# Optimization experiments

Measured on AMD Instinct MI355X. Metric: run time of the kernel, lower is better.

The kernel has to match this reference:

```python
import jax, jax.numpy as jnp
import numpy as np

# Model hyperparams (match init_kwargs)
B, T, CIN, COUT = 4, 12, 4, 4
P = 16; HIMG = WIMG = 256; HP = WP = 16
D = 384; L = 4; DFF = 4 * D; MAXG = 0.3
CPLX = jnp.complex64

# NOTE: RiemannianCliffordConv2d / TemporalPropagator / FluxTracker / basis /
# encoder / decoder sources were not provided; they are reconstructed here as
# faithful-structure surrogates: plain conv2d for the Clifford conv, complex
# linear eigen-basis encode/decode, exp-decay scan operators, complex FFN,
# patch-embed conv encoder and per-patch linear decoder. sde_mode='ode' so the
# stochastic branch is skipped, matching the explicit guard in the source.

def _ln(x, g, b):
    m = x.mean(-1, keepdims=True)
    v = jnp.var(x, axis=-1, keepdims=True)
    return (x - m) * jax.lax.rsqrt(v + 1e-5) * g + b

def _conv(x, w, b, stride, pad):
    y = jax.lax.conv_general_dilated(x, w, (stride, stride), pad,
                                     dimension_numbers=('NCHW', 'OIHW', 'NCHW'))
    return y + b[None, :, None, None]

def _pscan(A, X):
    # first-order linear recurrence h_t = A_t*h_{t-1} + X_t via associative scan over axis=1
    def comb(l, r):
        al, xl = l; ar, xr = r
        return al * ar, xl * ar + xr
    return jax.lax.associative_scan(comb, (A, X), axis=1)[1]

def _cgelu(z):
    return jax.nn.gelu(z.real) + 1j * jax.nn.gelu(z.imag)

def _model(x, dt, enc_w, enc_b, ns_g, ns_b, cw, cb, nt_g, nt_b,
           E_re, E_im, Ei_re, Ei_im, lam_flux, Ws_re, Ws_im, Wg, nu, omega,
           w1_re, w1_im, w2_re, w2_im, dec_w, dec_b):
    Bx, Tx = x.shape[0], x.shape[1]
    # ---- encoder: patch-embed conv -> complex latent (B,T,D,HP,WP)
    xf = x.reshape(Bx * Tx, CIN, HIMG, WIMG)
    e = _conv(xf, enc_w, enc_b, P, 'VALID')              # (BT, 2D, HP, WP)
    zr, zi = jnp.split(e, 2, axis=1)
    z = (zr + 1j * zi).astype(CPLX).reshape(Bx, Tx, D, HP, WP)
    for i in range(L):
        E = E_re[i] + 1j * E_im[i]
        Ei = Ei_re[i] + 1j * Ei_im[i]
        Ws = Ws_re[i] + 1j * Ws_im[i]
        W1 = w1_re[i] + 1j * w1_im[i]
        W2 = w2_re[i] + 1j * w2_im[i]
        # ---- _apply_spatial (residual Clifford conv on stacked re/im)
        xflat = z.reshape(Bx * Tx, D, HP, WP)
        xr2 = jnp.concatenate([xflat.real, xflat.imag], axis=1)   # (BT,2D,H,W)
        xn = jnp.transpose(xr2, (0, 2, 3, 1))
        xn = _ln(xn, ns_g[i], ns_b[i])
        xn = jnp.transpose(xn, (0, 3, 1, 2))
        xs = _conv(xn, cw[i], cb[i], 1, 'SAME')
        sre, sim = jnp.split(xs, 2, axis=1)
        xflat = xflat + (sre + 1j * sim)
        z = xflat.reshape(Bx, Tx, D, HP, WP)
        # ---- eigen-basis encode
        xp = jnp.transpose(z, (0, 1, 3, 4, 2))                    # (B,T,H,W,D)
        x_eig = jnp.einsum('bthwd,de->bthwe', xp, E)
        x_mean = x_eig.mean(axis=(2, 3))                          # (B,T,D)
        # ---- flux tracker scan (states start at zero => flux_prev term vanishes)
        a = jnp.exp(-jax.nn.softplus(lam_flux[i])[None, None] * dt[..., None])
        A_flux = a.astype(CPLX)
        X_flux = x_mean * dt[..., None]
        flux = _pscan(A_flux, X_flux)                             # (B,T,D) complex
        source = jnp.einsum('btd,de->bte', flux, Ws)
        gate = jax.nn.sigmoid(flux.real * Wg[i][None, None])      # (B,T,D) real
        g = gate[:, :, None, None, :]
        forcing = x_eig * g + source[:, :, None, None, :] * (1.0 - g)
        # ---- transition operators and temporal pscan
        lam = jnp.clip(-jax.nn.softplus(nu[i]), -5.0, MAXG) + 1j * omega[i]  # (D,)
        op_decay = jnp.exp(lam[None, None] * dt[..., None])       # (B,T,D) complex
        op_forcing = (op_decay - 1.0) / lam
        u_t = forcing * op_forcing[:, :, None, None, :]           # (B,T,H,W,D)
        # h_prev is zero-initialized per _init_states => its t0 contribution is zero
        A_full = jnp.broadcast_to(op_decay[:, :, None, None, :], u_t.shape)
        u_out = _pscan(A_full, u_t)                               # (B,T,H,W,D)
        # ---- decode + temporal FFN residual
        decoded = jnp.einsum('bthwd,de->bthwe', u_out, Ei)
        dec5 = jnp.transpose(decoded, (0, 1, 4, 2, 3))            # (B,T,D,H,W)
        df = dec5.reshape(Bx * Tx, D, HP, WP)
        dr = jnp.concatenate([df.real, df.imag], axis=1)
        dn = _ln(jnp.transpose(dr, (0, 2, 3, 1)), nt_g[i], nt_b[i])
        dn = jnp.transpose(dn, (0, 3, 1, 2))
        nre, nim = jnp.split(dn, 2, axis=1)
        xcl = jnp.transpose(nre + 1j * nim, (0, 2, 3, 1))          # (BT,H,W,D)
        delta = jnp.einsum('bhwf,fd->bhwd', _cgelu(jnp.einsum('bhwd,df->bhwf', xcl, W1)), W2)
        delta = jnp.transpose(delta, (0, 3, 1, 2))
        x_out = (df + delta).reshape(Bx, Tx, D, HP, WP)
        z = z + x_out
    # ---- ensemble decoder (mean member): per-patch linear head + depth-to-space
    feats = jnp.concatenate([z.real, z.imag], axis=2)             # (B,T,2D,H,W)
    fl = jnp.transpose(feats, (0, 1, 3, 4, 2))                    # (B,T,H,W,2D)
    y = jnp.einsum('bthwc,oc->bthwo', fl, dec_w) + dec_b
    y = y.reshape(Bx, Tx, HP, WP, COUT, P, P)
    y = jnp.transpose(y, (0, 1, 4, 2, 5, 3, 6)).reshape(Bx, Tx, COUT, HP * P, WP * P)
    return y


def setup_inputs() -> dict:
    key = jax.random.key(0)
    ks = jax.random.split(key, 32)
    s = 0.02
    d = {}
    d['x'] = jax.random.normal(ks[0], (B, T, CIN, HIMG, WIMG), dtype=jnp.float32)
    d['dt'] = jax.random.uniform(ks[1], (B, T), minval=0.5, maxval=1.5, dtype=jnp.float32)
    d['enc_w'] = jax.random.normal(ks[2], (2 * D, CIN, P, P), dtype=jnp.float32) * s
    d['enc_b'] = jnp.zeros((2 * D,), jnp.float32)
    d['ns_g'] = jnp.ones((L, 2 * D), jnp.float32)
    d['ns_b'] = jnp.zeros((L, 2 * D), jnp.float32)
    d['cw'] = jax.random.normal(ks[3], (L, 2 * D, 2 * D, 3, 3), dtype=jnp.float32) * s
    d['cb'] = jnp.zeros((L, 2 * D), jnp.float32)
    d['nt_g'] = jnp.ones((L, 2 * D), jnp.float32)
    d['nt_b'] = jnp.zeros((L, 2 * D), jnp.float32)
    d['E_re'] = jax.random.normal(ks[4], (L, D, D), dtype=jnp.float32) * s
    d['E_im'] = jax.random.normal(ks[5], (L, D, D), dtype=jnp.float32) * s
    d['Ei_re'] = jax.random.normal(ks[6], (L, D, D), dtype=jnp.float32) * s
    d['Ei_im'] = jax.random.normal(ks[7], (L, D, D), dtype=jnp.float32) * s
    d['lam_flux'] = jax.random.normal(ks[8], (L, D), dtype=jnp.float32)
    d['Ws_re'] = jax.random.normal(ks[9], (L, D, D), dtype=jnp.float32) * s
    d['Ws_im'] = jax.random.normal(ks[10], (L, D, D), dtype=jnp.float32) * s
    d['Wg'] = jax.random.normal(ks[11], (L, D), dtype=jnp.float32)
    d['nu'] = jax.random.normal(ks[12], (L, D), dtype=jnp.float32)
    d['omega'] = jax.random.normal(ks[13], (L, D), dtype=jnp.float32) * 0.5
    d['w1_re'] = jax.random.normal(ks[14], (L, D, DFF), dtype=jnp.float32) * s
    d['w1_im'] = jax.random.normal(ks[15], (L, D, DFF), dtype=jnp.float32) * s
    d['w2_re'] = jax.random.normal(ks[16], (L, DFF, D), dtype=jnp.float32) * s
    d['w2_im'] = jax.random.normal(ks[17], (L, DFF, D), dtype=jnp.float32) * s
    d['dec_w'] = jax.random.normal(ks[18], (COUT * P * P, 2 * D), dtype=jnp.float32) * s
    d['dec_b'] = jnp.zeros((COUT * P * P,), jnp.float32)
    return d


def reference(x, dt, enc_w, enc_b, ns_g, ns_b, cw, cb, nt_g, nt_b,
              E_re, E_im, Ei_re, Ei_im, lam_flux, Ws_re, Ws_im, Wg, nu, omega,
              w1_re, w1_im, w2_re, w2_im, dec_w, dec_b):
    return _model(x, dt, enc_w, enc_b, ns_g, ns_b, cw, cb, nt_g, nt_b,
                  E_re, E_im, Ei_re, Ei_im, lam_flux, Ws_re, Ws_im, Wg, nu, omega,
                  w1_re, w1_im, w2_re, w2_im, dec_w, dec_b)
```

## Files before the change

kernel.cpp:

```cpp
#include <hip/hip_runtime.h>
#include <cstddef>
#include <cstdint>

typedef unsigned short u16;
typedef short bf16x8 __attribute__((ext_vector_type(8)));
typedef float f32x4 __attribute__((ext_vector_type(4)));

__device__ __forceinline__ float gelu_tanh(float x) {
  float x3 = x * x * x;
  float t = tanhf(0.7978845608028654f * (x + 0.044715f * x3));
  return 0.5f * x * (1.0f + t);
}
__device__ __forceinline__ float softplus_f(float x) {
  return (x > 20.0f) ? x : log1pf(expf(x));
}
__device__ __forceinline__ u16 f2bf(float f) {
  uint32_t u = __float_as_uint(f);
  uint32_t r = (u + 0x7fffu + ((u >> 16) & 1u)) >> 16;
  return (u16)r;
}
__device__ __forceinline__ float bf2f(u16 v) {
  return __uint_as_float(((uint32_t)v) << 16);
}

__device__ __forceinline__ void gload16(const u16* g, u16* l) {
  __builtin_amdgcn_global_load_lds(
      (const __attribute__((address_space(1))) void*)g,
      (__attribute__((address_space(3))) void*)l, 16, 0, 0);
}

template <int TN, int MODE>
__global__ __launch_bounds__(256) void gemm_kernel(
    const u16* __restrict__ A, const u16* __restrict__ Bt, int K, int ldc,
    float* __restrict__ Cf, u16* __restrict__ Cb,
    const float* __restrict__ bias, const u16* __restrict__ Db) {
  static_assert(TN == 64, "192x64 tile only");
  __shared__ u16 As[2][192 * 32];
  __shared__ u16 Bs[2][64 * 32];
  const int m0 = blockIdx.x * 192, n0 = blockIdx.y * 64;
  const int tid = threadIdx.x;
  const int lane = tid & 63, w = tid >> 6;
  const int lane15 = lane & 15, quad = lane >> 4;
  const int r0 = lane >> 2, e0 = (lane & 3) * 8;

  const u16* ag0 = A + (size_t)(m0 + w * 48 + r0) * K + e0;
  const u16* ag1 = ag0 + (size_t)16 * K;
  const u16* ag2 = ag0 + (size_t)32 * K;
  const u16* bg0 = Bt + (size_t)(n0 + w * 16 + r0) * K + e0;

  f32x4 acc[3][4] = {};
  const int abase = (w * 48 + lane15) * 32 + quad * 8;
  const int bbase = lane15 * 32 + quad * 8;

  for (int k0 = 0; k0 < K; k0 += 64) {
#pragma unroll
    for (int p = 0; p < 2; ++p) {
      const int kk = k0 + 32 * p;
      gload16(ag0 + kk, &As[p][(w * 48) * 32]);
      gload16(ag1 + kk, &As[p][(w * 48 + 16) * 32]);
      gload16(ag2 + kk, &As[p][(w * 48 + 32) * 32]);
      gload16(bg0 + kk, &Bs[p][(w * 16) * 32]);
    }
    __syncthreads();
#pragma unroll
    for (int p = 0; p < 2; ++p) {
      bf16x8 af[3], bf[4];
#pragma unroll
      for (int i = 0; i < 3; ++i) af[i] = *(const bf16x8*)&As[p][abase + i * 16 * 32];
#pragma unroll
      for (int j = 0; j < 4; ++j) bf[j] = *(const bf16x8*)&Bs[p][bbase + j * 16 * 32];
#pragma unroll
      for (int i = 0; i < 3; ++i)
#pragma unroll
        for (int j = 0; j < 4; ++j)
          acc[i][j] = __builtin_amdgcn_mfma_f32_16x16x32_bf16(af[i], bf[j], acc[i][j], 0, 0, 0);
    }
    __syncthreads();
  }

  const int mw = m0 + w * 48;
#pragma unroll
  for (int i = 0; i < 3; ++i) {
#pragma unroll
    for (int j = 0; j < 4; ++j) {
      const int col = n0 + j * 16 + lane15;
#pragma unroll
      for (int r = 0; r < 4; ++r) {
        const int row = mw + i * 16 + quad * 4 + r;
        const float v = acc[i][j][r];
        const size_t idx = (size_t)row * ldc + col;
        if (MODE == 0) {
          Cf[idx] = v;
        } else if (MODE == 1) {
          Cb[idx] = f2bf(gelu_tanh(v));
        } else if (MODE == 2) {
          Cf[idx] += v;
        } else if (MODE == 3) {
          const int frame = row >> 8, pix = row & 255;
          const int hp = pix >> 4, wp = pix & 15;
          const int co = col >> 8, p1 = (col >> 4) & 15, p2 = col & 15;
          Cf[(((size_t)frame * 4 + co) * 256 + hp * 16 + p1) * 256 + wp * 16 + p2] = v + bias[col];
        } else if (MODE == 4) {
          Cf[idx] += v + bf2f(Db[idx]);
        } else if (MODE == 5) {
          const float nz = Cf[idx] + v;
          Cf[idx] = nz;
          Cb[idx] = f2bf(nz);
        } else if (MODE == 6) {
          Cb[idx] = f2bf(v);
        }
      }
    }
  }
}

__global__ __launch_bounds__(256) void conv_mfma_kernel(
    const u16* __restrict__ xnp, const u16* __restrict__ Btc,
    const float* __restrict__ cbias,
    float* __restrict__ z, u16* __restrict__ zb) {
  __shared__ u16 As[2][4 * 3 * 18 * 32];
  __shared__ u16 Bs[2][3 * 64 * 32];
  const int m0 = blockIdx.x * 192, n0 = blockIdx.y * 64;
  const int tid = threadIdx.x;
  const int lane = tid & 63, w = tid >> 6;
  const int lane15 = lane & 15, quad = lane >> 4;
  const int r0 = lane >> 2, e0 = (lane & 3) * 8;

  int fhp[3];
#pragma unroll
  for (int s = 0; s < 3; ++s) {
    const int rA = m0 + w * 48 + s * 16;
    fhp[s] = (rA >> 8) * 324 + ((rA & 255) >> 4) * 18;
  }
  const u16* bgt = Btc + (size_t)(n0 + w * 16 + r0) * 6912 + e0;

  f32x4 acc[3][4] = {};
  const int aseg = w * 3 * 18 * 32;

  for (int dy = 0; dy < 3; ++dy) {
    const u16* asrc[3];
#pragma unroll
    for (int s = 0; s < 3; ++s)
      asrc[s] = xnp + ((size_t)(fhp[s] + dy * 18 + r0)) * 768 + e0;
    const u16* bsrc = bgt + dy * 3 * 768;

    for (int kc = 0; kc < 768; kc += 64) {
#pragma unroll
      for (int p = 0; p < 2; ++p) {
        const int kk = kc + 32 * p;
#pragma unroll
        for (int s = 0; s < 3; ++s) {
          gload16(asrc[s] + kk, &As[p][aseg + s * 18 * 32]);
          gload16(asrc[s] + kk + 2 * 768, &As[p][aseg + s * 18 * 32 + 2 * 32]);
        }
#pragma unroll
        for (int dx = 0; dx < 3; ++dx)
          gload16(bsrc + dx * 768 + kk, &Bs[p][(dx * 64 + w * 16) * 32]);
      }
      __syncthreads();
#pragma unroll
      for (int p = 0; p < 2; ++p) {
#pragma unroll
        for (int dx = 0; dx < 3; ++dx) {
          bf16x8 af[3], bf[4];
#pragma unroll
          for (int i = 0; i < 3; ++i)
            af[i] = *(const bf16x8*)&As[p][aseg + (i * 18 + lane15 + dx) * 32 + quad * 8];
#pragma unroll
          for (int j = 0; j < 4; ++j)
            bf[j] = *(const bf16x8*)&Bs[p][(dx * 64 + j * 16 + lane15) * 32 + quad * 8];
#pragma unroll
          for (int i = 0; i < 3; ++i)
#pragma unroll
            for (int j = 0; j < 4; ++j)
              acc[i][j] = __builtin_amdgcn_mfma_f32_16x16x32_bf16(af[i], bf[j], acc[i][j], 0, 0, 0);
        }
      }
      __syncthreads();
    }
  }

  const int mw = m0 + w * 48;
#pragma unroll
  for (int i = 0; i < 3; ++i) {
#pragma unroll
    for (int j = 0; j < 4; ++j) {
      const int col = n0 + j * 16 + lane15;
      const float bv = cbias[col];
#pragma unroll
      for (int r = 0; r < 4; ++r) {
        const int row = mw + i * 16 + quad * 4 + r;
        const size_t idx = (size_t)row * 768 + col;
        const float nz = z[idx] + acc[i][j][r] + bv;
        z[idx] = nz;
        zb[idx] = f2bf(nz);
      }
    }
  }
}

__global__ __launch_bounds__(256) void encoder_mfma_kernel(
    const float* __restrict__ x, const float* __restrict__ ew,
    const float* __restrict__ eb, float* __restrict__ z) {
  __shared__ u16 As[128 * 32];
  __shared__ u16 Bs[128 * 32];
  const int m0 = blockIdx.x * 128, n0 = blockIdx.y * 128;
  const int tid = threadIdx.x;
  const int lane = tid & 63, w = tid >> 6;
  const int lane15 = lane & 15, quad = lane >> 4;
  const int srow = tid >> 1, half = tid & 1;
  const int arow = m0 + srow;
  const int frame = arow >> 8, pix = arow & 255, hh = pix >> 4, ww = pix & 15;

  f32x4 acc[4][4] = {};
  const int wy = w >> 1, wx = w & 1;
  const int ar_base = (wy * 64 + lane15) * 32 + quad * 8;
  const int br_base = (wx * 64 + lane15) * 32 + quad * 8;

  for (int k0 = 0; k0 < 1024; k0 += 32) {
    const int gk = k0 + half * 16;
    const int c = gk >> 8, ph = (gk >> 4) & 15;
    const float* ax = x + (((size_t)(frame * 4 + c) * 256 + hh * 16 + ph) * 256 + ww * 16);
    const float* bx = ew + (size_t)(n0 + srow) * 1024 + gk;
    u16 ta[16], tb[16];
#pragma unroll
    for (int j = 0; j < 4; ++j) {
      const float4 va = *(const float4*)(ax + j * 4);
      const float4 vb = *(const float4*)(bx + j * 4);
      ta[j * 4 + 0] = f2bf(va.x); ta[j * 4 + 1] = f2bf(va.y);
      ta[j * 4 + 2] = f2bf(va.z); ta[j * 4 + 3] = f2bf(va.w);
      tb[j * 4 + 0] = f2bf(vb.x); tb[j * 4 + 1] = f2bf(vb.y);
      tb[j * 4 + 2] = f2bf(vb.z); tb[j * 4 + 3] = f2bf(vb.w);
    }
    __syncthreads();
    *(uint4*)&As[srow * 32 + half * 16] = *(uint4*)ta;
    *(uint4*)&As[srow * 32 + half * 16 + 8] = *(uint4*)(ta + 8);
    *(uint4*)&Bs[srow * 32 + half * 16] = *(uint4*)tb;
    *(uint4*)&Bs[srow * 32 + half * 16 + 8] = *(uint4*)(tb + 8);
    __syncthreads();
    bf16x8 af[4], bfv[4];
#pragma unroll
    for (int i = 0; i < 4; ++i) af[i] = *(const bf16x8*)&As[ar_base + i * 16 * 32];
#pragma unroll
    for (int j = 0; j < 4; ++j) bfv[j] = *(const bf16x8*)&Bs[br_base + j * 16 * 32];
#pragma unroll
    for (int i = 0; i < 4; ++i)
#pragma unroll
      for (int j = 0; j < 4; ++j)
        acc[i][j] = __builtin_amdgcn_mfma_f32_16x16x32_bf16(af[i], bfv[j], acc[i][j], 0, 0, 0);
  }

  const int mw = m0 + wy * 64, nw = n0 + wx * 64;
#pragma unroll
  for (int i = 0; i < 4; ++i)
#pragma unroll
    for (int j = 0; j < 4; ++j) {
      const int col = nw + j * 16 + lane15;
      const float bv = eb[col];
#pragma unroll
      for (int r = 0; r < 4; ++r) {
        const int row = mw + i * 16 + quad * 4 + r;
        z[(size_t)row * 768 + col] = acc[i][j][r] + bv;
      }
    }
}

__global__ __launch_bounds__(256) void expand_kernel(
    const float* __restrict__ Wre, const float* __restrict__ Wim,
    int ldw, int Kc, int Nc, u16* __restrict__ Wt) {
  __shared__ float tile[32][33];
  const int k0 = blockIdx.x * 32, n0 = blockIdx.y * 32;
  const bool khi = k0 >= Kc, nhi = n0 >= Nc;
  const float* src = (khi != nhi) ? Wim : Wre;
  const float sgn = (!nhi && khi) ? -1.0f : 1.0f;
  const int sk = k0 - (khi ? Kc : 0), sn = n0 - (nhi ? Nc : 0);
  const int c = threadIdx.x & 31, r8 = threadIdx.x >> 5;
  for (int r = r8; r < 32; r += 8)
    tile[r][c] = src[(size_t)(sk + r) * ldw + sn + c];
  __syncthreads();
  const int twoK = 2 * Kc;
  for (int r = r8; r < 32; r += 8)
    Wt[(size_t)(n0 + r) * twoK + k0 + c] = f2bf(sgn * tile[c][r]);
}

__global__ __launch_bounds__(256) void reorder_cw_kernel(
    const float* __restrict__ cwl, u16* __restrict__ Btc) {
  __shared__ float buf[6912];
  const int o = blockIdx.x;
  const float* src = cwl + (size_t)o * 6912;
  for (int i = threadIdx.x; i < 6912; i += 256) buf[i] = src[i];
  __syncthreads();
  u16* dst = Btc + (size_t)o * 6912;
  for (int i = threadIdx.x; i < 6912; i += 256) {
    const int tap = i / 768, cc = i - tap * 768;
    dst[i] = f2bf(buf[cc * 9 + tap]);
  }
}

__global__ __launch_bounds__(256) void cast_bf16_kernel(
    const float* __restrict__ in, u16* __restrict__ out, int n) {
  const int g = blockIdx.x * 256 + threadIdx.x;
  if (g < n) out[g] = f2bf(in[g]);
}

__global__ __launch_bounds__(192) void ln_kernel(
    const float* __restrict__ in, const float* __restrict__ g,
    const float* __restrict__ b, u16* __restrict__ out) {
  const int row = blockIdx.x, tid = threadIdx.x;
  const float4 v = *(const float4*)(in + (size_t)row * 768 + tid * 4);
  float s = v.x + v.y + v.z + v.w;
  float q = v.x * v.x + v.y * v.y + v.z * v.z + v.w * v.w;
#pragma unroll
  for (int off = 32; off > 0; off >>= 1) {
    s += __shfl_down(s, off);
    q += __shfl_down(q, off);
  }
  __shared__ float rs[3], rq[3];
  if ((tid & 63) == 0) { rs[tid >> 6] = s; rq[tid >> 6] = q; }
  __syncthreads();
  const float S = rs[0] + rs[1] + rs[2], Q = rq[0] + rq[1] + rq[2];
  const float mean = S * (1.0f / 768.0f);
  const float inv = rsqrtf(Q * (1.0f / 768.0f) - mean * mean + 1e-5f);
  const float4 gv = *(const float4*)(g + tid * 4);
  const float4 bv = *(const float4*)(b + tid * 4);
  u16 p[4];
  p[0] = f2bf((v.x - mean) * inv * gv.x + bv.x);
  p[1] = f2bf((v.y - mean) * inv * gv.y + bv.y);
  p[2] = f2bf((v.z - mean) * inv * gv.z + bv.z);
  p[3] = f2bf((v.w - mean) * inv * gv.w + bv.w);
  const int f = row >> 8, pp = row & 255, h = pp >> 4, ww = pp & 15;
  const size_t base = ((size_t)f * 324 + (h + 1) * 18 + ww + 1) * 768;
  *(uint2*)(out + base + tid * 4) = *(uint2*)p;
}

__global__ __launch_bounds__(192) void ln_bf_kernel(
    const u16* __restrict__ in, const float* __restrict__ g,
    const float* __restrict__ b, u16* __restrict__ out) {
  const int row = blockIdx.x, tid = threadIdx.x;
  const uint2 raw = *(const uint2*)(in + (size_t)row * 768 + tid * 4);
  const u16* rp = (const u16*)&raw;
  const float v0 = bf2f(rp[0]), v1 = bf2f(rp[1]), v2 = bf2f(rp[2]), v3 = bf2f(rp[3]);
  float s = v0 + v1 + v2 + v3;
  float q = v0 * v0 + v1 * v1 + v2 * v2 + v3 * v3;
#pragma unroll
  for (int off = 32; off > 0; off >>= 1) {
    s += __shfl_down(s, off);
    q += __shfl_down(q, off);
  }
  __shared__ float rs[3], rq[3];
  if ((tid & 63) == 0) { rs[tid >> 6] = s; rq[tid >> 6] = q; }
  __syncthreads();
  const float S = rs[0] + rs[1] + rs[2], Q = rq[0] + rq[1] + rq[2];
  const float mean = S * (1.0f / 768.0f);
  const float inv = rsqrtf(Q * (1.0f / 768.0f) - mean * mean + 1e-5f);
  const float4 gv = *(const float4*)(g + tid * 4);
  const float4 bv = *(const float4*)(b + tid * 4);
  u16 p[4];
  p[0] = f2bf((v0 - mean) * inv * gv.x + bv.x);
  p[1] = f2bf((v1 - mean) * inv * gv.y + bv.y);
  p[2] = f2bf((v2 - mean) * inv * gv.z + bv.z);
  p[3] = f2bf((v3 - mean) * inv * gv.w + bv.w);
  *(uint2*)(out + (size_t)row * 768 + tid * 4) = *(uint2*)p;
}

__global__ __launch_bounds__(768) void mean_kernel(
    const u16* __restrict__ eig, float* __restrict__ mr, float* __restrict__ mi) {
  const int f = blockIdx.x, c = threadIdx.x;
  const u16* p = eig + (size_t)f * 256 * 768 + c;
  float s0 = 0.f, s1 = 0.f, s2 = 0.f, s3 = 0.f;
  for (int px = 0; px < 256; px += 4) {
    s0 += bf2f(p[(size_t)px * 768]);
    s1 += bf2f(p[(size_t)(px + 1) * 768]);
    s2 += bf2f(p[(size_t)(px + 2) * 768]);
    s3 += bf2f(p[(size_t)(px + 3) * 768]);
  }
  const float tot = (s0 + s1 + s2 + s3) * (1.0f / 256.0f);
  if (c < 384) mr[f * 384 + c] = tot;
  else         mi[f * 384 + c - 384] = tot;
}

__global__ __launch_bounds__(384) void flux_kernel(
    const float* __restrict__ dt, const float* __restrict__ lamf,
    const float* __restrict__ nu, const float* __restrict__ omega,
    const float* __restrict__ mr, const float* __restrict__ mi,
    float* __restrict__ fluxr, float* __restrict__ fluxi,
    float* __restrict__ opdr, float* __restrict__ opdi,
    float* __restrict__ opfr, float* __restrict__ opfi) {
  const int b = blockIdx.x;
  const int d = threadIdx.x;
  const float sp = softplus_f(lamf[d]);
  float lre = -softplus_f(nu[d]);
  lre = fmaxf(lre, -5.0f);
  const float lim = omega[d];
  const float den = lre * lre + lim * lim;
  float fr = 0.f, fi = 0.f;
  for (int t = 0; t < 12; ++t) {
    const float dtv = dt[b * 12 + t];
    const int idx = (b * 12 + t) * 384 + d;
    const float A = expf(-sp * dtv);
    fr = A * fr + mr[idx] * dtv;
    fi = A * fi + mi[idx] * dtv;
    fluxr[idx] = fr; fluxi[idx] = fi;
    const float ed = expf(lre * dtv);
    const float odr = ed * cosf(lim * dtv);
    const float odi = ed * sinf(lim * dtv);
    opdr[idx] = odr; opdi[idx] = odi;
    const float nr_ = odr - 1.0f, ni_ = odi;
    opfr[idx] = (nr_ * lre + ni_ * lim) / den;
    opfi[idx] = (ni_ * lre - nr_ * lim) / den;
  }
}

#define SBM 64
#define SBN 64
#define SBK 32
__global__ __launch_bounds__(256) void cgemm_src_kernel(
    const float* __restrict__ Ar, const float* __restrict__ Ai, int lda,
    const float* __restrict__ Wr, const float* __restrict__ Wi, int ldw,
    const float* __restrict__ Wg,
    float* __restrict__ G, float* __restrict__ SGr, float* __restrict__ SGi,
    int ldc, int M, int K) {
  __shared__ float Asr[SBK][SBM], Asi[SBK][SBM];
  __shared__ float Wsr[SBK][SBN], Wsi[SBK][SBN];
  const int m0 = blockIdx.x * SBM;
  const int n0 = blockIdx.y * SBN;
  const int tid = threadIdx.x;
  const int tn = tid & 15, tm = tid >> 4;
  float accr[4][4] = {}, acci[4][4] = {};
  for (int k0 = 0; k0 < K; k0 += SBK) {
    for (int s = tid; s < 512; s += 256) {
      {
        int r = s >> 3, kk = (s & 7) << 2;
        int row = m0 + r;
        float4 vr = {0.f, 0.f, 0.f, 0.f}, vi = {0.f, 0.f, 0.f, 0.f};
        if (row < M) {
          vr = *(const float4*)(Ar + (size_t)row * lda + k0 + kk);
          vi = *(const float4*)(Ai + (size_t)row * lda + k0 + kk);
        }
        Asr[kk + 0][r] = vr.x; Asr[kk + 1][r] = vr.y; Asr[kk + 2][r] = vr.z; Asr[kk + 3][r] = vr.w;
        Asi[kk + 0][r] = vi.x; Asi[kk + 1][r] = vi.y; Asi[kk + 2][r] = vi.z; Asi[kk + 3][r] = vi.w;
      }
      {
        int wr_ = s >> 4, wc = (s & 15) << 2;
        *(float4*)&Wsr[wr_][wc] = *(const float4*)(Wr + (size_t)(k0 + wr_) * ldw + n0 + wc);
        *(float4*)&Wsi[wr_][wc] = *(const float4*)(Wi + (size_t)(k0 + wr_) * ldw + n0 + wc);
      }
    }
    __syncthreads();
#pragma unroll
    for (int kk = 0; kk < SBK; ++kk) {
      float4 ar4 = *(const float4*)&Asr[kk][tm << 2];
      float4 ai4 = *(const float4*)&Asi[kk][tm << 2];
      float4 wr4 = *(const float4*)&Wsr[kk][tn << 2];
      float4 wi4 = *(const float4*)&Wsi[kk][tn << 2];
      float ar[4] = {ar4.x, ar4.y, ar4.z, ar4.w};
      float ai[4] = {ai4.x, ai4.y, ai4.z, ai4.w};
      float wr[4] = {wr4.x, wr4.y, wr4.z, wr4.w};
      float wi[4] = {wi4.x, wi4.y, wi4.z, wi4.w};
#pragma unroll
      for (int i = 0; i < 4; ++i)
#pragma unroll
        for (int j = 0; j < 4; ++j) {
          accr[i][j] = fmaf(ar[i], wr[j], accr[i][j]);
          accr[i][j] = fmaf(-ai[i], wi[j], accr[i][j]);
          acci[i][j] = fmaf(ar[i], wi[j], acci[i][j]);
          acci[i][j] = fmaf(ai[i], wr[j], acci[i][j]);
        }
    }
    __syncthreads();
  }
#pragma unroll
  for (int i = 0; i < 4; ++i) {
    int row = m0 + (tm << 2) + i;
    if (row >= M) continue;
#pragma unroll
    for (int j = 0; j < 4; ++j) {
      int col = n0 + (tn << 2) + j;
      size_t idx = (size_t)row * ldc + col;
      const float gate = 1.0f / (1.0f + expf(-Ar[idx] * Wg[col]));
      G[idx] = gate;
      SGr[idx] = accr[i][j] * (1.0f - gate);
      SGi[idx] = acci[i][j] * (1.0f - gate);
    }
  }
}

__global__ __launch_bounds__(256) void pscan_fused_kernel(
    const u16* __restrict__ eig,
    const float* __restrict__ Gv,
    const float* __restrict__ SGr, const float* __restrict__ SGi,
    const float* __restrict__ opfr, const float* __restrict__ opfi,
    const float* __restrict__ opdr, const float* __restrict__ opdi,
    u16* __restrict__ ub) {
  const int g = blockIdx.x * 256 + threadIdx.x;
  if (g >= 4 * 256 * 384) return;
  const int d = g % 384;
  const int pix = (g / 384) & 255;
  const int b = g / (384 * 256);
  float ur = 0.f, ui = 0.f;
  for (int t = 0; t < 12; ++t) {
    const int frame = b * 12 + t;
    const size_t idx = ((size_t)frame * 256 + pix) * 768 + d;
    const int fidx = frame * 384 + d;
    const float G = Gv[fidx];
    const float fr = bf2f(eig[idx]) * G + SGr[fidx];
    const float fi = bf2f(eig[idx + 384]) * G + SGi[fidx];
    const float pr = opfr[fidx], pi = opfi[fidx];
    const float utr = fr * pr - fi * pi;
    const float uti = fr * pi + fi * pr;
    const float ar = opdr[fidx], ai = opdi[fidx];
    const float nr = ar * ur - ai * ui + utr;
    const float ni = ar * ui + ai * ur + uti;
    ub[idx] = f2bf(nr); ub[idx + 384] = f2bf(ni);
    ur = nr; ui = ni;
  }
}

extern "C" void kernel_launch(void* const* d_in, const int* in_sizes, int n_in,
                              void* d_out, int out_size, void* d_ws, size_t ws_size,
                              hipStream_t stream) {
  const float* x        = (const float*)d_in[0];
  const float* dt       = (const float*)d_in[1];
  const float* enc_w    = (const float*)d_in[2];
  const float* enc_b    = (const float*)d_in[3];
  const float* ns_g     = (const float*)d_in[4];
  const float* ns_b     = (const float*)d_in[5];
  const float* cw       = (const float*)d_in[6];
  const float* cb       = (const float*)d_in[7];
  const float* nt_g     = (const float*)d_in[8];
  const float* nt_b     = (const float*)d_in[9];
  const float* E_re     = (const float*)d_in[10];
  const float* E_im     = (const float*)d_in[11];
  const float* Ei_re    = (const float*)d_in[12];
  const float* Ei_im    = (const float*)d_in[13];
  const float* lam_flux = (const float*)d_in[14];
  const float* Ws_re    = (const float*)d_in[15];
  const float* Ws_im    = (const float*)d_in[16];
  const float* Wg       = (const float*)d_in[17];
  const float* nu       = (const float*)d_in[18];
  const float* omega    = (const float*)d_in[19];
  const float* w1_re    = (const float*)d_in[20];
  const float* w1_im    = (const float*)d_in[21];
  const float* w2_re    = (const float*)d_in[22];
  const float* w2_im    = (const float*)d_in[23];
  const float* dec_w    = (const float*)d_in[24];
  const float* dec_b    = (const float*)d_in[25];
  float* out = (float*)d_out;

  const size_t NPF = 12288ull * 768;
  const size_t XNP = 48ull * 324 * 768;
  const size_t SM = 48ull * 384;

  float* z    = (float*)d_ws;
  float* eigf = z + NPF;
  float* dff  = eigf + NPF;
  u16* xnp    = (u16*)(dff + NPF);
  u16* Btc    = xnp + XNP;
  u16* Et     = Btc + 5308416;
  u16* Eit    = Et + 589824;
  u16* W1t    = Eit + 589824;
  u16* W2t    = W1t + 2359296;
  u16* dwt    = W2t + 2359296;
  float* sm   = (float*)(dwt + 786432);
  float* mr    = sm;            float* mi    = mr + SM;
  float* fluxr = mi + SM;       float* fluxi = fluxr + SM;
  float* opdr  = fluxi + SM;    float* opdi  = opdr + SM;
  float* opfr  = opdi + SM;     float* opfi  = opfr + SM;
  float* Gv    = opfi + SM;     float* SGr   = Gv + SM;
  float* SGi   = SGr + SM;

  const size_t need = ((char*)(SGi + SM)) - ((char*)d_ws);
  if (ws_size < need) return;

  u16* eig_b = (u16*)eigf;
  u16* h1b   = (u16*)eigf;
  u16* df_b  = (u16*)dff;
  u16* zbuf  = (u16*)dff + NPF;

  cast_bf16_kernel<<<(786432 + 255) / 256, 256, 0, stream>>>(dec_w, dwt, 786432);
  encoder_mfma_kernel<<<dim3(96, 6), 256, 0, stream>>>(x, enc_w, enc_b, z);

  for (int l = 0; l < 4; ++l) {
    const size_t DD = 384ull * 384, DF = 384ull * 1536;
    hipMemsetAsync(xnp, 0, XNP * sizeof(u16), stream);
    reorder_cw_kernel<<<768, 256, 0, stream>>>(cw + (size_t)l * 768 * 768 * 9, Btc);
    expand_kernel<<<dim3(24, 24), 256, 0, stream>>>(E_re + l * DD, E_im + l * DD, 384, 384, 384, Et);
    expand_kernel<<<dim3(24, 24), 256, 0, stream>>>(Ei_re + l * DD, Ei_im + l * DD, 384, 384, 384, Eit);
    for (int ch = 0; ch < 2; ++ch) {
      expand_kernel<<<dim3(24, 48), 256, 0, stream>>>(
          w1_re + l * DF + ch * 768, w1_im + l * DF + ch * 768, 1536, 384, 768, W1t + (size_t)ch * 1179648);
      expand_kernel<<<dim3(48, 24), 256, 0, stream>>>(
          w2_re + l * DF + (size_t)ch * 768 * 384, w2_im + l * DF + (size_t)ch * 768 * 384, 384, 768, 384,
          W2t + (size_t)ch * 1179648);
    }

    ln_kernel<<<12288, 192, 0, stream>>>(z, ns_g + l * 768, ns_b + l * 768, xnp);
    conv_mfma_kernel<<<dim3(64, 12), 256, 0, stream>>>(xnp, Btc, cb + l * 768, z, zbuf);
    gemm_kernel<64, 6><<<dim3(64, 12), 256, 0, stream>>>(zbuf, Et, 768, 768, nullptr, eig_b, nullptr, nullptr);
    mean_kernel<<<48, 768, 0, stream>>>(eig_b, mr, mi);
    flux_kernel<<<4, 384, 0, stream>>>(dt, lam_flux + l * 384, nu + l * 384, omega + l * 384,
                                       mr, mi, fluxr, fluxi, opdr, opdi, opfr, opfi);
    cgemm_src_kernel<<<dim3(1, 6), 256, 0, stream>>>(
        fluxr, fluxi, 384, Ws_re + l * DD, Ws_im + l * DD, 384,
        Wg + l * 384, Gv, SGr, SGi, 384, 48, 384);
    pscan_fused_kernel<<<1536, 256, 0, stream>>>(eig_b, Gv, SGr, SGi, opfr, opfi, opdr, opdi, xnp);
    gemm_kernel<64, 6><<<dim3(64, 12), 256, 0, stream>>>(xnp, Eit, 768, 768, nullptr, df_b, nullptr, nullptr);
    ln_bf_kernel<<<12288, 192, 0, stream>>>(df_b, nt_g + l * 768, nt_b + l * 768, xnp);
    for (int ch = 0; ch < 2; ++ch) {
      gemm_kernel<64, 1><<<dim3(64, 24), 256, 0, stream>>>(
          xnp, W1t + (size_t)ch * 1179648, 768, 1536, nullptr, h1b, nullptr, nullptr);
      if (ch == 0) {
        gemm_kernel<64, 4><<<dim3(64, 12), 256, 0, stream>>>(
            h1b, W2t, 1536, 768, z, nullptr, nullptr, df_b);
      } else if (l < 3) {
        gemm_kernel<64, 2><<<dim3(64, 12), 256, 0, stream>>>(
            h1b, W2t + 1179648, 1536, 768, z, nullptr, nullptr, nullptr);
      } else {
        gemm_kernel<64, 5><<<dim3(64, 12), 256, 0, stream>>>(
            h1b, W2t + 1179648, 1536, 768, z, zbuf, nullptr, nullptr);
      }
    }
  }

  gemm_kernel<64, 3><<<dim3(64, 16), 256, 0, stream>>>(zbuf, dwt, 768, 0, out, nullptr, dec_b, nullptr);
}
```

Baseline: 2.512 ms.

## Merge weight-prep kernels, hoist padding memset, retile encoder and contiguous conv loads

The six per-layer weight expand launches and the conv weight reorder are merged into one 3D-grid mega kernel, which cuts launch count. The padded LN buffer memset is hoisted out of the layer loop by routing the pscan output and the second LN output to other scratch buffers, so the zero padding border stays intact. The encoder GEMM is retiled to 192x64 blocks with a 12x more uniform load pattern. The conv kernel adds a fast path that loads contiguous padded rows when a warp's 48 rows stay inside one frame, which reduces the number of global-to-LDS loads. Risks are buffer aliasing between ub/xn and eig_b/zbuf, and a mega grid that launches many empty blocks.

```diff
diff --git a/kernel.cpp b/kernel.cpp
--- a/kernel.cpp
+++ b/kernel.cpp
@@ -118,7 +118,7 @@
     const u16* __restrict__ xnp, const u16* __restrict__ Btc,
     const float* __restrict__ cbias,
     float* __restrict__ z, u16* __restrict__ zb) {
-  __shared__ u16 As[2][4 * 3 * 18 * 32];
+  __shared__ u16 As[2][4 * 54 * 32];
   __shared__ u16 Bs[2][3 * 64 * 32];
   const int m0 = blockIdx.x * 192, n0 = blockIdx.y * 64;
   const int tid = threadIdx.x;
@@ -126,18 +126,24 @@
   const int lane15 = lane & 15, quad = lane >> 4;
   const int r0 = lane >> 2, e0 = (lane & 3) * 8;
 
+  const int rowA0 = m0 + w * 48;
+  const int q = (rowA0 >> 4) & 15;
+  const bool fast = (q <= 13);
+  const long long cbase = ((long long)(rowA0 >> 8) * 324 + q * 18) * 768;
+
   int fhp[3];
 #pragma unroll
   for (int s = 0; s < 3; ++s) {
-    const int rA = m0 + w * 48 + s * 16;
+    const int rA = rowA0 + s * 16;
     fhp[s] = (rA >> 8) * 324 + ((rA & 255) >> 4) * 18;
   }
   const u16* bgt = Btc + (size_t)(n0 + w * 16 + r0) * 6912 + e0;
 
   f32x4 acc[3][4] = {};
-  const int aseg = w * 3 * 18 * 32;
+  const int aseg = w * 54 * 32;
 
   for (int dy = 0; dy < 3; ++dy) {
+    const u16* afast = xnp + cbase + (size_t)dy * (18 * 768) + (size_t)r0 * 768 + e0;
     const u16* asrc[3];
 #pragma unroll
     for (int s = 0; s < 3; ++s)
@@ -148,10 +154,17 @@
 #pragma unroll
       for (int p = 0; p < 2; ++p) {
         const int kk = kc + 32 * p;
-#pragma unroll
-        for (int s = 0; s < 3; ++s) {
-          gload16(asrc[s] + kk, &As[p][aseg + s * 18 * 32]);
-          gload16(asrc[s] + kk + 2 * 768, &As[p][aseg + s * 18 * 32 + 2 * 32]);
+        if (fast) {
+          gload16(afast + kk, &As[p][aseg]);
+          gload16(afast + kk + 16 * 768, &As[p][aseg + 16 * 32]);
+          gload16(afast + kk + 32 * 768, &As[p][aseg + 32 * 32]);
+          gload16(afast + kk + 38 * 768, &As[p][aseg + 38 * 32]);
+        } else {
+#pragma unroll
+          for (int s = 0; s < 3; ++s) {
+            gload16(asrc[s] + kk, &As[p][aseg + s * 18 * 32]);
+            gload16(asrc[s] + kk + 2 * 768, &As[p][aseg + s * 18 * 32 + 2 * 32]);
+          }
         }
 #pragma unroll
         for (int dx = 0; dx < 3; ++dx)
@@ -202,60 +215,64 @@
 __global__ __launch_bounds__(256) void encoder_mfma_kernel(
     const float* __restrict__ x, const float* __restrict__ ew,
     const float* __restrict__ eb, float* __restrict__ z) {
-  __shared__ u16 As[128 * 32];
-  __shared__ u16 Bs[128 * 32];
-  const int m0 = blockIdx.x * 128, n0 = blockIdx.y * 128;
+  __shared__ u16 As[192 * 32];
+  __shared__ u16 Bs[64 * 32];
+  const int m0 = blockIdx.x * 192, n0 = blockIdx.y * 64;
   const int tid = threadIdx.x;
   const int lane = tid & 63, w = tid >> 6;
   const int lane15 = lane & 15, quad = lane >> 4;
-  const int srow = tid >> 1, half = tid & 1;
-  const int arow = m0 + srow;
-  const int frame = arow >> 8, pix = arow & 255, hh = pix >> 4, ww = pix & 15;
-
-  f32x4 acc[4][4] = {};
-  const int wy = w >> 1, wx = w & 1;
-  const int ar_base = (wy * 64 + lane15) * 32 + quad * 8;
-  const int br_base = (wx * 64 + lane15) * 32 + quad * 8;
+
+  f32x4 acc[3][4] = {};
+  const int abase = (w * 48 + lane15) * 32 + quad * 8;
+  const int bbase = lane15 * 32 + quad * 8;
 
   for (int k0 = 0; k0 < 1024; k0 += 32) {
-    const int gk = k0 + half * 16;
-    const int c = gk >> 8, ph = (gk >> 4) & 15;
-    const float* ax = x + (((size_t)(frame * 4 + c) * 256 + hh * 16 + ph) * 256 + ww * 16);
-    const float* bx = ew + (size_t)(n0 + srow) * 1024 + gk;
-    u16 ta[16], tb[16];
-#pragma unroll
-    for (int j = 0; j < 4; ++j) {
-      const float4 va = *(const float4*)(ax + j * 4);
-      const float4 vb = *(const float4*)(bx + j * 4);
-      ta[j * 4 + 0] = f2bf(va.x); ta[j * 4 + 1] = f2bf(va.y);
-      ta[j * 4 + 2] = f2bf(va.z); ta[j * 4 + 3] = f2bf(va.w);
-      tb[j * 4 + 0] = f2bf(vb.x); tb[j * 4 + 1] = f2bf(vb.y);
-      tb[j * 4 + 2] = f2bf(vb.z); tb[j * 4 + 3] = f2bf(vb.w);
-    }
     __syncthreads();
-    *(uint4*)&As[srow * 32 + half * 16] = *(uint4*)ta;
-    *(uint4*)&As[srow * 32 + half * 16 + 8] = *(uint4*)(ta + 8);
-    *(uint4*)&Bs[srow * 32 + half * 16] = *(uint4*)tb;
-    *(uint4*)&Bs[srow * 32 + half * 16 + 8] = *(uint4*)(tb + 8);
+#pragma unroll
+    for (int pass = 0; pass < 3; ++pass) {
+      const int id = tid + pass * 256;
+      const int row = id >> 2, kc8 = (id & 3) * 8;
+      const int arow = m0 + row;
+      const int frame = arow >> 8, pix = arow & 255, hh = pix >> 4, ww = pix & 15;
+      const int gk = k0 + kc8;
+      const int c = gk >> 8, ph = (gk >> 4) & 15, pw = gk & 15;
+      const float* ax = x + (((size_t)(frame * 4 + c) * 256 + hh * 16 + ph) * 256 + ww * 16 + pw);
+      const float4 v0 = *(const float4*)ax;
+      const float4 v1 = *(const float4*)(ax + 4);
+      u16 t8[8];
+      t8[0] = f2bf(v0.x); t8[1] = f2bf(v0.y); t8[2] = f2bf(v0.z); t8[3] = f2bf(v0.w);
+      t8[4] = f2bf(v1.x); t8[5] = f2bf(v1.y); t8[6] = f2bf(v1.z); t8[7] = f2bf(v1.w);
+      *(uint4*)&As[row * 32 + kc8] = *(uint4*)t8;
+    }
+    {
+      const int row = tid >> 2, kc8 = (tid & 3) * 8;
+      const float* bx = ew + (size_t)(n0 + row) * 1024 + k0 + kc8;
+      const float4 v0 = *(const float4*)bx;
+      const float4 v1 = *(const float4*)(bx + 4);
+      u16 t8[8];
+      t8[0] = f2bf(v0.x); t8[1] = f2bf(v0.y); t8[2] = f2bf(v0.z); t8[3] = f2bf(v0.w);
+      t8[4] = f2bf(v1.x); t8[5] = f2bf(v1.y); t8[6] = f2bf(v1.z); t8[7] = f2bf(v1.w);
+      *(uint4*)&Bs[row * 32 + kc8] = *(uint4*)t8;
+    }
     __syncthreads();
-    bf16x8 af[4], bfv[4];
-#pragma unroll
-    for (int i = 0; i < 4; ++i) af[i] = *(const bf16x8*)&As[ar_base + i * 16 * 32];
-#pragma unroll
-    for (int j = 0; j < 4; ++j) bfv[j] = *(const bf16x8*)&Bs[br_base + j * 16 * 32];
-#pragma unroll
-    for (int i = 0; i < 4; ++i)
+    bf16x8 af[3], bfv[4];
+#pragma unroll
+    for (int i = 0; i < 3; ++i) af[i] = *(const bf16x8*)&As[abase + i * 16 * 32];
+#pragma unroll
+    for (int j = 0; j < 4; ++j) bfv[j] = *(const bf16x8*)&Bs[bbase + j * 16 * 32];
+#pragma unroll
+    for (int i = 0; i < 3; ++i)
 #pragma unroll
       for (int j = 0; j < 4; ++j)
         acc[i][j] = __builtin_amdgcn_mfma_f32_16x16x32_bf16(af[i], bfv[j], acc[i][j], 0, 0, 0);
   }
 
-  const int mw = m0 + wy * 64, nw = n0 + wx * 64;
-#pragma unroll
-  for (int i = 0; i < 4; ++i)
+  const int mw = m0 + w * 48;
+#pragma unroll
+  for (int i = 0; i < 3; ++i)
 #pragma unroll
     for (int j = 0; j < 4; ++j) {
-      const int col = nw + j * 16 + lane15;
+      const int col = n0 + j * 16 + lane15;
       const float bv = eb[col];
 #pragma unroll
       for (int r = 0; r < 4; ++r) {
@@ -265,10 +282,48 @@
     }
 }
 
-__global__ __launch_bounds__(256) void expand_kernel(
-    const float* __restrict__ Wre, const float* __restrict__ Wim,
-    int ldw, int Kc, int Nc, u16* __restrict__ Wt) {
-  __shared__ float tile[32][33];
+__global__ __launch_bounds__(256) void mega_expand_kernel(
+    const float* __restrict__ E_re, const float* __restrict__ E_im,
+    const float* __restrict__ Ei_re, const float* __restrict__ Ei_im,
+    const float* __restrict__ w1_re, const float* __restrict__ w1_im,
+    const float* __restrict__ w2_re, const float* __restrict__ w2_im,
+    const float* __restrict__ cwl,
+    u16* __restrict__ Et, u16* __restrict__ Eit,
+    u16* __restrict__ W1t, u16* __restrict__ W2t, u16* __restrict__ Btc) {
+  __shared__ float shbuf[6912];
+  const int zz = blockIdx.z;
+
+  if (zz == 6) {
+    const int o = blockIdx.y * 48 + blockIdx.x;
+    if (o >= 768) return;
+    const float* src = cwl + (size_t)o * 6912;
+    for (int i = threadIdx.x; i < 6912; i += 256) shbuf[i] = src[i];
+    __syncthreads();
+    u16* dst = Btc + (size_t)o * 6912;
+    for (int i = threadIdx.x; i < 6912; i += 256) {
+      const int tap = i / 768, cc = i - tap * 768;
+      dst[i] = f2bf(shbuf[cc * 9 + tap]);
+    }
+    return;
+  }
+
+  const float *Wre, *Wim;
+  int ldw, Kc, Nc, gx, gy;
+  u16* Wt;
+  const size_t DF = 384ull * 1536;
+  switch (zz) {
+    case 0:  Wre = E_re;  Wim = E_im;  ldw = 384;  Kc = 384; Nc = 384; Wt = Et;  gx = 24; gy = 24; break;
+    case 1:  Wre = Ei_re; Wim = Ei_im; ldw = 384;  Kc = 384; Nc = 384; Wt = Eit; gx = 24; gy = 24; break;
+    case 2:  Wre = w1_re; Wim = w1_im; ldw = 1536; Kc = 384; Nc = 768; Wt = W1t; gx = 24; gy = 48; break;
+    case 3:  Wre = w1_re + 768; Wim = w1_im + 768; ldw = 1536; Kc = 384; Nc = 768;
+             Wt = W1t + 1179648; gx = 24; gy = 48; break;
+    case 4:  Wre = w2_re; Wim = w2_im; ldw = 384;  Kc = 768; Nc = 384; Wt = W2t; gx = 48; gy = 24; break;
+    default: Wre = w2_re + DF / 2; Wim = w2_im + DF / 2; ldw = 384; Kc = 768; Nc = 384;
+             Wt = W2t + 1179648; gx = 48; gy = 24; break;
+  }
+  if ((int)blockIdx.x >= gx || (int)blockIdx.y >= gy) return;
+
+  float (*tile)[33] = (float(*)[33])shbuf;
   const int k0 = blockIdx.x * 32, n0 = blockIdx.y * 32;
   const bool khi = k0 >= Kc, nhi = n0 >= Nc;
   const float* src = (khi != nhi) ? Wim : Wre;
@@ -281,20 +336,6 @@
   const int twoK = 2 * Kc;
   for (int r = r8; r < 32; r += 8)
     Wt[(size_t)(n0 + r) * twoK + k0 + c] = f2bf(sgn * tile[c][r]);
-}
-
-__global__ __launch_bounds__(256) void reorder_cw_kernel(
-    const float* __restrict__ cwl, u16* __restrict__ Btc) {
-  __shared__ float buf[6912];
-  const int o = blockIdx.x;
-  const float* src = cwl + (size_t)o * 6912;
-  for (int i = threadIdx.x; i < 6912; i += 256) buf[i] = src[i];
-  __syncthreads();
-  u16* dst = Btc + (size_t)o * 6912;
-  for (int i = threadIdx.x; i < 6912; i += 256) {
-    const int tap = i / 768, cc = i - tap * 768;
-    dst[i] = f2bf(buf[cc * 9 + tap]);
-  }
 }
 
 __global__ __launch_bounds__(256) void cast_bf16_kernel(
@@ -573,26 +614,22 @@
   if (ws_size < need) return;
 
   u16* eig_b = (u16*)eigf;
+  u16* ub    = (u16*)eigf + NPF;
   u16* h1b   = (u16*)eigf;
   u16* df_b  = (u16*)dff;
   u16* zbuf  = (u16*)dff + NPF;
+  u16* xn    = (u16*)dff + NPF;
 
   cast_bf16_kernel<<<(786432 + 255) / 256, 256, 0, stream>>>(dec_w, dwt, 786432);
-  encoder_mfma_kernel<<<dim3(96, 6), 256, 0, stream>>>(x, enc_w, enc_b, z);
+  hipMemsetAsync(xnp, 0, XNP * sizeof(u16), stream);
+  encoder_mfma_kernel<<<dim3(64, 12), 256, 0, stream>>>(x, enc_w, enc_b, z);
 
   for (int l = 0; l < 4; ++l) {
     const size_t DD = 384ull * 384, DF = 384ull * 1536;
-    hipMemsetAsync(xnp, 0, XNP * sizeof(u16), stream);
-    reorder_cw_kernel<<<768, 256, 0, stream>>>(cw + (size_t)l * 768 * 768 * 9, Btc);
-    expand_kernel<<<dim3(24, 24), 256, 0, stream>>>(E_re + l * DD, E_im + l * DD, 384, 384, 384, Et);
-    expand_kernel<<<dim3(24, 24), 256, 0, stream>>>(Ei_re + l * DD, Ei_im + l * DD, 384, 384, 384, Eit);
-    for (int ch = 0; ch < 2; ++ch) {
-      expand_kernel<<<dim3(24, 48), 256, 0, stream>>>(
-          w1_re + l * DF + ch * 768, w1_im + l * DF + ch * 768, 1536, 384, 768, W1t + (size_t)ch * 1179648);
-      expand_kernel<<<dim3(48, 24), 256, 0, stream>>>(
-          w2_re + l * DF + (size_t)ch * 768 * 384, w2_im + l * DF + (size_t)ch * 768 * 384, 384, 768, 384,
-          W2t + (size_t)ch * 1179648);
-    }
+    mega_expand_kernel<<<dim3(48, 48, 7), 256, 0, stream>>>(
+        E_re + l * DD, E_im + l * DD, Ei_re + l * DD, Ei_im + l * DD,
+        w1_re + l * DF, w1_im + l * DF, w2_re + l * DF, w2_im + l * DF,
+        cw + (size_t)l * 768 * 768 * 9, Et, Eit, W1t, W2t, Btc);
 
     ln_kernel<<<12288, 192, 0, stream>>>(z, ns_g + l * 768, ns_b + l * 768, xnp);
     conv_mfma_kernel<<<dim3(64, 12), 256, 0, stream>>>(xnp, Btc, cb + l * 768, z, zbuf);
@@ -603,12 +640,12 @@
     cgemm_src_kernel<<<dim3(1, 6), 256, 0, stream>>>(
         fluxr, fluxi, 384, Ws_re + l * DD, Ws_im + l * DD, 384,
         Wg + l * 384, Gv, SGr, SGi, 384, 48, 384);
-    pscan_fused_kernel<<<1536, 256, 0, stream>>>(eig_b, Gv, SGr, SGi, opfr, opfi, opdr, opdi, xnp);
-    gemm_kernel<64, 6><<<dim3(64, 12), 256, 0, stream>>>(xnp, Eit, 768, 768, nullptr, df_b, nullptr, nullptr);
-    ln_bf_kernel<<<12288, 192, 0, stream>>>(df_b, nt_g + l * 768, nt_b + l * 768, xnp);
+    pscan_fused_kernel<<<1536, 256, 0, stream>>>(eig_b, Gv, SGr, SGi, opfr, opfi, opdr, opdi, ub);
+    gemm_kernel<64, 6><<<dim3(64, 12), 256, 0, stream>>>(ub, Eit, 768, 768, nullptr, df_b, nullptr, nullptr);
+    ln_bf_kernel<<<12288, 192, 0, stream>>>(df_b, nt_g + l * 768, nt_b + l * 768, xn);
     for (int ch = 0; ch < 2; ++ch) {
       gemm_kernel<64, 1><<<dim3(64, 24), 256, 0, stream>>>(
-          xnp, W1t + (size_t)ch * 1179648, 768, 1536, nullptr, h1b, nullptr, nullptr);
+          xn, W1t + (size_t)ch * 1179648, 768, 1536, nullptr, h1b, nullptr, nullptr);
       if (ch == 0) {
         gemm_kernel<64, 4><<<dim3(64, 12), 256, 0, stream>>>(
             h1b, W2t, 1536, 768, z, nullptr, nullptr, df_b);
```

After: 2.472 ms. Within noise of the previous version (-1.6%).
